# Kernel tuning notes

Measured on AMD Instinct MI355X. Metric: run time of the kernel, lower is better.

The kernel has to match this reference:

```python
import jax, jax.numpy as jnp
import numpy as np

N_FFT = 1024
HOP = 256
F_BINS = N_FFT // 2 + 1  # 513


def _make_dft_kernel():
    # torch.hann_window(N) is periodic: 0.5*(1 - cos(2*pi*k/N))
    window = 0.5 * (1.0 - np.cos(2.0 * np.pi * np.arange(N_FFT) / N_FFT))
    # rfft of identity, transposed -> (F, n_fft), then apply window along time axis
    dftm = np.fft.rfft(np.eye(N_FFT)).T * window[None, :]  # complex (F, n_fft)
    # view_as_real + rearrange 'f n ri -> (ri f) n': real block first, imag block second
    kernel = np.concatenate([dftm.real, dftm.imag], axis=0)  # (2F, n_fft)
    return jnp.asarray(kernel, dtype=jnp.float32)


def setup_inputs() -> dict:
    key = jax.random.key(0)
    signal = jax.random.normal(key, (16, 262144), dtype=jnp.float32)
    kernel = _make_dft_kernel()  # (1026, 1024) fixed windowed-DFT matrix (buffer)
    return {"signal": signal, "kernel": kernel}


def reference(signal, kernel):
    # center=True: reflect-pad by n_fft//2 on both sides
    pad = N_FFT // 2
    x = jnp.pad(signal, ((0, 0), (pad, pad)), mode="reflect")  # (B, L)
    B, L = x.shape
    n_frames = (L - N_FFT) // HOP + 1
    # im2col framing: (n_frames, n_fft) gather indices
    idx = jnp.arange(n_frames)[:, None] * HOP + jnp.arange(N_FFT)[None, :]
    frames = x[:, idx]  # (B, n_frames, n_fft)
    # conv1d as GEMM: (B, 2F, n_frames)
    out = jnp.einsum("btn,cn->bct", frames, kernel)
    # rearrange '(ri f) n -> f n ri' with ri outer
    out = out.reshape(B, 2, F_BINS, n_frames)
    return jnp.transpose(out, (0, 2, 3, 1))  # (B, F, n_frames, 2)
```

## Files before the change

### kernel.cpp

```cpp
#include <hip/hip_runtime.h>
#include <hip/hip_bf16.h>
#include <cstdint>


#define HOP 256
#define NFFT 1024
#define FB 513
#define NT 1025
#define NBATCH 16
#define MCH 1026
#define MP 1152
#define SIGLEN 262144
#define SIGP 263168
#define BM 128
#define BT 128
#define BK 64

typedef __attribute__((ext_vector_type(8))) short short8;
typedef __attribute__((ext_vector_type(4))) float f32x4;
typedef unsigned int u32;

__device__ __forceinline__ unsigned short f2bf(float f) {
  u32 u = __float_as_uint(f);
  u = (u + 0x7FFFu + ((u >> 16) & 1u)) >> 16;
  return (unsigned short)u;
}

__global__ __launch_bounds__(256) void prep_A(const float* __restrict__ kern,
                                              unsigned short* __restrict__ A) {
  size_t i8 = ((size_t)blockIdx.x * 256 + threadIdx.x) * 8;
  int row = (int)(i8 >> 10);
  int col = (int)(i8 & 1023);
  short8 v = {0, 0, 0, 0, 0, 0, 0, 0};
  if (row < MCH) {
    int f = row >> 1, ri = row & 1;
    int src_row = ri * FB + f;
    const float* s = kern + ((size_t)src_row << 10) + col;
#pragma unroll
    for (int e = 0; e < 8; ++e) v[e] = (short)f2bf(s[e]);
  }
  *(short8*)(A + i8) = v;
}

__global__ __launch_bounds__(256) void prep_S(const float* __restrict__ sig,
                                              unsigned short* __restrict__ S) {
  size_t i8 = ((size_t)blockIdx.x * 256 + threadIdx.x) * 8;
  int b = (int)(i8 / SIGP);
  int i = (int)(i8 - (size_t)b * SIGP);
  const float* sb = sig + (size_t)b * SIGLEN;
  short8 v;
#pragma unroll
  for (int e = 0; e < 8; ++e) {
    int j = i + e - 512;
    j = (j < 0) ? -j : j;
    j = (j >= SIGLEN) ? (2 * SIGLEN - 2 - j) : j;
    v[e] = (short)f2bf(sb[j]);
  }
  *(short8*)(S + i8) = v;
}

__device__ __forceinline__ void async16(void* lds, const void* g) {
  __builtin_amdgcn_global_load_lds(
      (const __attribute__((address_space(1))) u32*)g,
      (__attribute__((address_space(3))) u32*)lds, 16, 0, 0);
}

__global__ __launch_bounds__(256, 4) void stft_mm(const unsigned short* __restrict__ A,
                                                  const unsigned short* __restrict__ S,
                                                  float* __restrict__ out) {
  __shared__ __align__(16) short sA[BM * BK];
  __shared__ __align__(16) short sB[BT * BK];

  const int tid = threadIdx.x;
  const int lane = tid & 63;
  const int wid = tid >> 6;
  const int wc = wid >> 1;
  const int wt = wid & 1;
  const int lr = lane & 15;
  const int g16 = lane >> 4;

  const int bid = blockIdx.x;
  const int wg = (bid & 7) * 162 + (bid >> 3);
  const int mt = wg % 9;
  const int tb = wg / 9;
  const int tt = tb % 9;
  const int b  = tb / 9;

  const int c0 = mt * BM;
  const int t0 = tt * BT;

  const unsigned short* Sb = S + (size_t)b * SIGP;

  f32x4 acc[4][4] = {};

  for (int kt = 0; kt < 16; ++kt) {
    const int n0 = kt * BK;
#pragma unroll
    for (int j = 0; j < 4; ++j) {
      const u32 G = (u32)(wid * 256 + j * 64);
      u32 p = (G + (u32)lane) * 16u;
      u32 q = p ^ (((p >> 7) & 7u) << 4);
      int row = (int)(q >> 7);
      int kk = (int)((q & 127u) >> 1);
      const unsigned short* src = A + ((size_t)(c0 + row) << 10) + (n0 + kk);
      async16((char*)sA + (size_t)G * 16u, src);
    }
#pragma unroll
    for (int j = 0; j < 4; ++j) {
      const u32 G = (u32)(wid * 256 + j * 64);
      u32 p = (G + (u32)lane) * 16u;
      u32 q = p ^ (((p >> 7) & 7u) << 4);
      int trow = (int)(q >> 7);
      int kk = (int)((q & 127u) >> 1);
      int s = (t0 + trow) * HOP + n0 + kk;
      s = (s > SIGP - 8) ? (SIGP - 8) : s;
      async16((char*)sB + (size_t)G * 16u, Sb + s);
    }
    __syncthreads();

#pragma unroll
    for (int h = 0; h < 2; ++h) {
      short8 af[4], bfv[4];
#pragma unroll
      for (int mi = 0; mi < 4; ++mi) {
        int cl = wc * 64 + mi * 16 + lr;
        u32 a = (u32)(cl * 128 + h * 64 + g16 * 16);
        a ^= ((u32)(cl & 7) << 4);
        af[mi] = *(const short8*)((const char*)sA + a);
      }
#pragma unroll
      for (int ni = 0; ni < 4; ++ni) {
        int tl = wt * 64 + ni * 16 + lr;
        u32 a = (u32)(tl * 128 + h * 64 + g16 * 16);
        a ^= ((u32)(tl & 7) << 4);
        bfv[ni] = *(const short8*)((const char*)sB + a);
      }
#pragma unroll
      for (int mi = 0; mi < 4; ++mi)
#pragma unroll
        for (int ni = 0; ni < 4; ++ni)
          acc[mi][ni] =
              __builtin_amdgcn_mfma_f32_16x16x32_bf16(af[mi], bfv[ni], acc[mi][ni], 0, 0, 0);
    }
    __syncthreads();
  }

#pragma unroll
  for (int mi = 0; mi < 4; ++mi) {
    const int cb = c0 + wc * 64 + mi * 16 + g16 * 4;
    const int f0 = cb >> 1;
#pragma unroll
    for (int ni = 0; ni < 4; ++ni) {
      const int t = t0 + wt * 64 + ni * 16 + lr;
      if (t < NT) {
        if (f0 < FB) {
          *(float2*)(out + ((((size_t)b * FB + f0) * NT + t) << 1)) =
              make_float2(acc[mi][ni][0], acc[mi][ni][1]);
        }
        if (f0 + 1 < FB) {
          *(float2*)(out + ((((size_t)b * FB + f0 + 1) * NT + t) << 1)) =
              make_float2(acc[mi][ni][2], acc[mi][ni][3]);
        }
      }
    }
  }
}

extern "C" void kernel_launch(void* const* d_in, const int* in_sizes, int n_in,
                              void* d_out, int out_size, void* d_ws, size_t ws_size,
                              hipStream_t stream) {
  const float* sig = (const float*)d_in[0];
  const float* kern = (const float*)d_in[1];
  float* out = (float*)d_out;

  unsigned short* wsA = (unsigned short*)d_ws;
  unsigned short* wsS = wsA + (size_t)MP * NFFT;

  prep_A<<<dim3(MP * NFFT / 8 / 256), 256, 0, stream>>>(kern, wsA);
  prep_S<<<dim3(NBATCH * SIGP / 8 / 256), 256, 0, stream>>>(sig, wsS);
  stft_mm<<<dim3(9 * 9 * NBATCH), 256, 0, stream>>>(wsA, wsS, out);
}
```

Before: 68.44 us.

## Stage shared signal window once in LDS and stream DFT matrix from global

Each block now loads one contiguous signal window covering its 64 frames into LDS once, using overlap between hop-spaced frames instead of re-gathering frame tiles per K step. The DFT weights are read directly from global memory into registers, with no per-K-step LDS staging and no barriers inside the loop. Tiles are reshaped to 256 channels by 64 frames, and the padded A buffer grows to 1280 rows. The intent is to cut LDS traffic and synchronisation, at the cost of uncoalesced, cache-dependent global loads for A with no software prefetch.

```diff
diff --git a/kernel.cpp b/kernel.cpp
--- a/kernel.cpp
+++ b/kernel.cpp
@@ -9,12 +9,14 @@
 #define NT 1025
 #define NBATCH 16
 #define MCH 1026
-#define MP 1152
+#define MP2 1280
 #define SIGLEN 262144
 #define SIGP 263168
-#define BM 128
-#define BT 128
-#define BK 64
+#define TW 64
+#define WSAMP 17152
+#define WGRAN 1072
+#undef WGRAN
+#define WGRAN 2144
 
 typedef __attribute__((ext_vector_type(8))) short short8;
 typedef __attribute__((ext_vector_type(4))) float f32x4;
@@ -68,72 +70,66 @@
 __global__ __launch_bounds__(256, 4) void stft_mm(const unsigned short* __restrict__ A,
                                                   const unsigned short* __restrict__ S,
                                                   float* __restrict__ out) {
-  __shared__ __align__(16) short sA[BM * BK];
-  __shared__ __align__(16) short sB[BT * BK];
+  __shared__ __align__(16) short sW[WSAMP];
 
   const int tid = threadIdx.x;
   const int lane = tid & 63;
   const int wid = tid >> 6;
-  const int wc = wid >> 1;
-  const int wt = wid & 1;
   const int lr = lane & 15;
   const int g16 = lane >> 4;
 
   const int bid = blockIdx.x;
-  const int wg = (bid & 7) * 162 + (bid >> 3);
-  const int mt = wg % 9;
-  const int tb = wg / 9;
-  const int tt = tb % 9;
-  const int b  = tb / 9;
+  const int wg = (bid & 7) * 170 + (bid >> 3);
+  const int bm = wg % 5;
+  const int r2 = wg / 5;
+  const int bt = r2 % 17;
+  const int b  = r2 / 17;
 
-  const int c0 = mt * BM;
-  const int t0 = tt * BT;
+  const int c0 = bm * 256;
+  const int t0 = bt * TW;
 
   const unsigned short* Sb = S + (size_t)b * SIGP;
+  const size_t w0 = (size_t)t0 * HOP;
+
+#pragma unroll
+  for (int i = 0; i < 9; ++i) {
+    const int base = i * 256 + wid * 64;
+    if (base < WGRAN) {
+      u32 p = (u32)(base + lane) * 16u;
+      u32 q = p ^ (((p >> 9) & 7u) << 4);
+      size_t src = w0 + (size_t)(q >> 1);
+      if (src > (size_t)(SIGP - 8)) src = SIGP - 8;
+      async16((char*)sW + (size_t)base * 16u, Sb + src);
+    }
+  }
+  __syncthreads();
+
+  const char* pA[4];
+#pragma unroll
+  for (int mi = 0; mi < 4; ++mi) {
+    int row = c0 + wid * 64 + mi * 16 + lr;
+    pA[mi] = (const char*)(A + ((size_t)row << 10)) + g16 * 16;
+  }
+  u32 bq[4];
+#pragma unroll
+  for (int ni = 0; ni < 4; ++ni) bq[ni] = (u32)((ni * 16 + lr) * 512 + g16 * 16);
 
   f32x4 acc[4][4] = {};
 
+#pragma unroll
   for (int kt = 0; kt < 16; ++kt) {
-    const int n0 = kt * BK;
-#pragma unroll
-    for (int j = 0; j < 4; ++j) {
-      const u32 G = (u32)(wid * 256 + j * 64);
-      u32 p = (G + (u32)lane) * 16u;
-      u32 q = p ^ (((p >> 7) & 7u) << 4);
-      int row = (int)(q >> 7);
-      int kk = (int)((q & 127u) >> 1);
-      const unsigned short* src = A + ((size_t)(c0 + row) << 10) + (n0 + kk);
-      async16((char*)sA + (size_t)G * 16u, src);
-    }
-#pragma unroll
-    for (int j = 0; j < 4; ++j) {
-      const u32 G = (u32)(wid * 256 + j * 64);
-      u32 p = (G + (u32)lane) * 16u;
-      u32 q = p ^ (((p >> 7) & 7u) << 4);
-      int trow = (int)(q >> 7);
-      int kk = (int)((q & 127u) >> 1);
-      int s = (t0 + trow) * HOP + n0 + kk;
-      s = (s > SIGP - 8) ? (SIGP - 8) : s;
-      async16((char*)sB + (size_t)G * 16u, Sb + s);
-    }
-    __syncthreads();
-
 #pragma unroll
     for (int h = 0; h < 2; ++h) {
+      const int koff = kt * 128 + h * 64;
       short8 af[4], bfv[4];
 #pragma unroll
-      for (int mi = 0; mi < 4; ++mi) {
-        int cl = wc * 64 + mi * 16 + lr;
-        u32 a = (u32)(cl * 128 + h * 64 + g16 * 16);
-        a ^= ((u32)(cl & 7) << 4);
-        af[mi] = *(const short8*)((const char*)sA + a);
-      }
+      for (int mi = 0; mi < 4; ++mi)
+        af[mi] = *(const short8*)(pA[mi] + koff);
 #pragma unroll
       for (int ni = 0; ni < 4; ++ni) {
-        int tl = wt * 64 + ni * 16 + lr;
-        u32 a = (u32)(tl * 128 + h * 64 + g16 * 16);
-        a ^= ((u32)(tl & 7) << 4);
-        bfv[ni] = *(const short8*)((const char*)sB + a);
+        u32 q = bq[ni] + (u32)koff;
+        u32 p = q ^ (((q >> 9) & 7u) << 4);
+        bfv[ni] = *(const short8*)((const char*)sW + p);
       }
 #pragma unroll
       for (int mi = 0; mi < 4; ++mi)
@@ -142,16 +138,15 @@
           acc[mi][ni] =
               __builtin_amdgcn_mfma_f32_16x16x32_bf16(af[mi], bfv[ni], acc[mi][ni], 0, 0, 0);
     }
-    __syncthreads();
   }
 
 #pragma unroll
   for (int mi = 0; mi < 4; ++mi) {
-    const int cb = c0 + wc * 64 + mi * 16 + g16 * 4;
+    const int cb = c0 + wid * 64 + mi * 16 + g16 * 4;
     const int f0 = cb >> 1;
 #pragma unroll
     for (int ni = 0; ni < 4; ++ni) {
-      const int t = t0 + wt * 64 + ni * 16 + lr;
+      const int t = t0 + ni * 16 + lr;
       if (t < NT) {
         if (f0 < FB) {
           *(float2*)(out + ((((size_t)b * FB + f0) * NT + t) << 1)) =
@@ -174,9 +169,9 @@
   float* out = (float*)d_out;
 
   unsigned short* wsA = (unsigned short*)d_ws;
-  unsigned short* wsS = wsA + (size_t)MP * NFFT;
+  unsigned short* wsS = wsA + (size_t)MP2 * NFFT;
 
-  prep_A<<<dim3(MP * NFFT / 8 / 256), 256, 0, stream>>>(kern, wsA);
+  prep_A<<<dim3(MP2 * NFFT / 8 / 256), 256, 0, stream>>>(kern, wsA);
   prep_S<<<dim3(NBATCH * SIGP / 8 / 256), 256, 0, stream>>>(sig, wsS);
-  stft_mm<<<dim3(9 * 9 * NBATCH), 256, 0, stream>>>(wsA, wsS, out);
+  stft_mm<<<dim3(5 * 17 * NBATCH), 256, 0, stream>>>(wsA, wsS, out);
 }
```

After: 129.8 us. +89.7%, slower.
